# Kernel tuning notes

Hardware: AMD Instinct MI355X
Metric: run time of the kernel (lower is better)

## Reference

```python
import jax, jax.numpy as jnp
import numpy as np

N = 4096       # nodes
E = 131072     # edges (avg degree 32)
IN_C = 512
HID = 512
OUT_C = 64
RANK = 64      # svd_q
N_DOM = 4
EPS = 1e-5     # BatchNorm eps


def setup_inputs() -> dict:
    key = jax.random.key(0)
    ks = jax.random.split(key, 12)
    x = jax.random.normal(ks[0], (N, IN_C), dtype=jnp.float32)
    row = jax.random.randint(ks[1], (E,), 0, N)
    off = jax.random.randint(ks[2], (E,), 1, N)
    col = (row + off) % N  # guarantee no pre-existing self loops
    edge_index = jnp.stack([row, col]).astype(jnp.int32)
    edge_weight = jax.random.uniform(ks[3], (E,), dtype=jnp.float32)
    y = jax.random.randint(ks[4], (N,), 0, N_DOM).astype(jnp.int32)
    W1 = jax.random.normal(ks[5], (IN_C, HID), dtype=jnp.float32) / np.sqrt(IN_C).astype(np.float32)
    b1 = jnp.zeros((HID,), jnp.float32)
    Wmu = jax.random.normal(ks[6], (HID, OUT_C), dtype=jnp.float32) / np.sqrt(HID).astype(np.float32)
    bmu = jnp.zeros((OUT_C,), jnp.float32)
    Wlv = jax.random.normal(ks[7], (HID, OUT_C), dtype=jnp.float32) / np.sqrt(HID).astype(np.float32)
    blv = jnp.zeros((OUT_C,), jnp.float32)
    gamma = jnp.ones((N_DOM, HID), jnp.float32)   # per-domain BN weight
    beta = jnp.zeros((N_DOM, HID), jnp.float32)   # per-domain BN bias
    return dict(x=x, edge_index=edge_index, edge_weight=edge_weight, y=y,
                W1=W1, b1=b1, Wmu=Wmu, bmu=bmu, Wlv=Wlv, blv=blv,
                gamma=gamma, beta=beta)


def _safe_rsqrt(deg):
    # PyG gcn_norm: deg^-0.5 with inf (and here non-positive) masked to 0
    safe = jnp.where(deg > 0, deg, 1.0)
    return jnp.where(deg > 0, 1.0 / jnp.sqrt(safe), 0.0)


def gcn_conv_edges(x, W, b, row, col, w, n):
    # GCNConv with edge weights: add remaining self loops (fill=1), symmetric norm
    loop = jnp.arange(n, dtype=row.dtype)
    row_f = jnp.concatenate([row, loop])
    col_f = jnp.concatenate([col, loop])
    w_f = jnp.concatenate([w, jnp.ones((n,), w.dtype)])
    deg = jax.ops.segment_sum(w_f, col_f, num_segments=n)
    dinv = _safe_rsqrt(deg)
    norm = dinv[row_f] * w_f * dinv[col_f]
    xw = x @ W                                   # [n, out]
    out = jax.ops.segment_sum(norm[:, None] * xw[row_f], col_f, num_segments=n)
    return out + b


def gcn_conv_dense(x, W, b, A):
    # Dense-adjacency GCNConv (reconstructed adjacency already has a diagonal,
    # so add_remaining_self_loops is a no-op). deg over target (col) index.
    deg = A.sum(axis=0)
    dinv = _safe_rsqrt(deg)
    Ahat = dinv[:, None] * A * dinv[None, :]     # [n, n] normalized
    return Ahat.T @ (x @ W) + b                  # aggregate at targets


def svd_lowrank_recon(A, q, niter=2):
    # torch.svd_lowrank-style randomized SVD, then U @ diag(s) @ V^T
    omega = jax.random.normal(jax.random.key(42), (A.shape[1], q), A.dtype)
    Qb = jnp.linalg.qr(A @ omega)[0]
    for _ in range(niter):
        Qb = jnp.linalg.qr(A.T @ Qb)[0]
        Qb = jnp.linalg.qr(A @ Qb)[0]
    B = Qb.T @ A                                 # [q, n]
    U, s, Vt = jnp.linalg.svd(B, full_matrices=False)
    return (Qb @ (U * s)) @ Vt                   # [n, n] low-rank reconstruction


def dsbn_relu(x, y, gamma, beta):
    # Domain-specific BatchNorm (training-mode batch stats per domain) + ReLU
    out = jnp.zeros_like(x)
    for i in range(N_DOM):
        m = (y == i)
        mf = m.astype(x.dtype)[:, None]
        cnt = jnp.maximum(mf.sum(), 1.0)
        mean = (x * mf).sum(0) / cnt
        var = (((x - mean) ** 2) * mf).sum(0) / cnt   # biased var, as BatchNorm
        xn = (x - mean) / jnp.sqrt(var + EPS) * gamma[i] + beta[i]
        out = jnp.where(m[:, None], xn, out)
    return jax.nn.relu(out)


def reference(x, edge_index, edge_weight, y, W1, b1, Wmu, bmu, Wlv, blv, gamma, beta):
    row, col = edge_index[0], edge_index[1]
    # ----- branch 1: original sparse graph -----
    h1 = dsbn_relu(gcn_conv_edges(x, W1, b1, row, col, edge_weight, N), y, gamma, beta)
    z_mean1 = gcn_conv_edges(h1, Wmu, bmu, row, col, edge_weight, N)
    z_log1 = gcn_conv_edges(h1, Wlv, blv, row, col, edge_weight, N)
    # ----- branch 2: SVD low-rank reconstructed (dense) graph -----
    A = jnp.zeros((N, N), x.dtype).at[row, col].add(edge_weight)  # coalesced COO
    A2 = svd_lowrank_recon(A, RANK)
    h2 = dsbn_relu(gcn_conv_dense(x, W1, b1, A2), y, gamma, beta)
    z_mean2 = gcn_conv_dense(h2, Wmu, bmu, A2)
    z_log2 = gcn_conv_dense(h2, Wlv, blv, A2)
    return (z_mean1, z_log1, z_mean2, z_log2)
```

## Files before the change

### kernel.cpp

```cpp
#include <hip/hip_runtime.h>
#include <hip/hip_bf16.h>


#define NN    4096
#define NEDG  131072
#define INC   512
#define HIDC  512
#define OUTC  64
#define RK    64
#define NDOM  4
#define EPSBN 1e-5f

typedef unsigned short ushortT;
typedef __attribute__((ext_vector_type(8))) short bf16x8;
typedef __attribute__((ext_vector_type(4))) float f32x4;

static inline int cdiv(int a, int b){ return (a + b - 1) / b; }

__device__ __forceinline__ float bf2f(unsigned u){ return __uint_as_float(u << 16); }

__global__ __launch_bounds__(256) void k_detect(const unsigned short* __restrict__ p,
                                                int* __restrict__ flag){
  int t = threadIdx.x;
  int cnt = 0;
  for (int i = t; i < 4096; i += 256){
    unsigned short v = p[2*i];
    int e = (v >> 7) & 0xFF;
    if (e >= 100 && e <= 140) cnt++;
  }
  __shared__ int sh[256];
  sh[t] = cnt; __syncthreads();
  for (int off = 128; off > 0; off >>= 1){ if (t < off) sh[t] += sh[t+off]; __syncthreads(); }
  if (t == 0) *flag = (sh[0] >= 2048) ? 0 : 1;
}

__device__ __forceinline__ float upc1(const void* s, int f, int off){
  return f ? ((const float*)s)[off]
           : __bfloat162float(((const __hip_bfloat16*)s)[off]);
}
__device__ __forceinline__ ushortT tobf(float v){
  __hip_bfloat16 h = __float2bfloat16(v);
  return *(ushortT*)&h;
}
#define SEG_X   2097152
#define SEG_W1  262144
#define SEG_W   131072
#define SEG_WMU 32768
#define SEG_GB  2048
#define SEG_B1  512
#define SEG_BO  64
#define OFF1 (SEG_X)
#define OFF2 (OFF1+SEG_W1)
#define OFF3 (OFF2+SEG_W)
#define OFF4 (OFF3+SEG_WMU)
#define OFF5 (OFF4+SEG_WMU)
#define OFF6 (OFF5+SEG_GB)
#define OFF7 (OFF6+SEG_GB)
#define OFF8 (OFF7+SEG_B1)
#define OFF9 (OFF8+SEG_BO)
#define OFFT (OFF9+SEG_BO)

__global__ __launch_bounds__(256) void k_upcast_all(
    const void* x, const void* W1, const void* w, const void* Wmu, const void* Wlv,
    const void* gm, const void* bt, const void* b1, const void* bmu, const void* blv,
    const int* __restrict__ isf32,
    float* dx, float* dW1, float* dw, float* dWmu, float* dWlv,
    float* dgm, float* dbt, float* db1, float* dbmu, float* dblv,
    ushortT* xbf, ushortT* W1bf, ushortT* Wmubf, ushortT* Wlvbf){
  int i = blockIdx.x*256 + threadIdx.x;
  if (i >= OFFT) return;
  int f = *isf32;
  if      (i < OFF1){ float v = upc1(x, f, i); dx[i] = v; xbf[i] = tobf(v); }
  else if (i < OFF2){ float v = upc1(W1, f, i - OFF1); dW1[i - OFF1] = v; W1bf[i - OFF1] = tobf(v); }
  else if (i < OFF3) dw  [i - OFF2] = upc1(w,   f, i - OFF2);
  else if (i < OFF4){ float v = upc1(Wmu, f, i - OFF3); dWmu[i - OFF3] = v; Wmubf[i - OFF3] = tobf(v); }
  else if (i < OFF5){ float v = upc1(Wlv, f, i - OFF4); dWlv[i - OFF4] = v; Wlvbf[i - OFF4] = tobf(v); }
  else if (i < OFF6) dgm [i - OFF5] = upc1(gm,  f, i - OFF5);
  else if (i < OFF7) dbt [i - OFF6] = upc1(bt,  f, i - OFF6);
  else if (i < OFF8) db1 [i - OFF7] = upc1(b1,  f, i - OFF7);
  else if (i < OFF9) dbmu[i - OFF8] = upc1(bmu, f, i - OFF8);
  else               dblv[i - OFF9] = upc1(blv, f, i - OFF9);
}

__global__ __launch_bounds__(256) void k_fill(float* d, float v, int n){
  int i = blockIdx.x*256 + threadIdx.x;
  if (i < n) d[i] = v;
}
__global__ __launch_bounds__(256) void k_filld(double* d, double v, int n){
  int i = blockIdx.x*256 + threadIdx.x;
  if (i < n) d[i] = v;
}
__global__ __launch_bounds__(256) void k_prep(float* deg, int* cntR, int* cntC, int* dcnt){
  int i = blockIdx.x*256 + threadIdx.x;
  if (i < NN){ deg[i] = 1.0f; cntR[i] = 0; cntC[i] = 0; }
  if (i < NDOM) dcnt[i] = 0;
}
__global__ __launch_bounds__(256) void k_f64to32x2(const double* __restrict__ s0, float* __restrict__ d0,
                                                   const double* __restrict__ s1, float* __restrict__ d1,
                                                   int n){
  int i = blockIdx.x*256 + threadIdx.x;
  if (i < n){ d0[i] = (float)s0[i]; d1[i] = (float)s1[i]; }
}

__global__ __launch_bounds__(256) void k_hist(const int* __restrict__ row, const int* __restrict__ col,
                                              const float* __restrict__ w, float* deg,
                                              int* cntR, int* cntC){
  int e = blockIdx.x*256 + threadIdx.x;
  if (e < NEDG){
    atomicAdd(&deg[col[e]], w[e]);
    atomicAdd(&cntR[row[e]], 1);
    atomicAdd(&cntC[col[e]], 1);
  }
}
__global__ __launch_bounds__(256) void k_dinv(const float* deg, float* dinv, int n){
  int i = blockIdx.x*256 + threadIdx.x;
  if (i < n){ float d = deg[i]; dinv[i] = (d > 0.f) ? 1.f/sqrtf(d) : 0.f; }
}
__global__ __launch_bounds__(256) void k_norm1(const int* __restrict__ row, const int* __restrict__ col,
                                               const float* __restrict__ w, const float* __restrict__ dinv,
                                               float* __restrict__ nrm){
  int e = blockIdx.x*256 + threadIdx.x;
  if (e < NEDG) nrm[e] = dinv[row[e]] * w[e] * dinv[col[e]];
}
__global__ __launch_bounds__(1024) void k_scan4096(const int* __restrict__ cnt,
                                                   int* __restrict__ ptr, int* __restrict__ pos){
  __shared__ int sh[1024];
  int t = threadIdx.x;
  int b = t*4;
  int a0 = cnt[b], a1 = cnt[b+1], a2 = cnt[b+2], a3 = cnt[b+3];
  sh[t] = a0 + a1 + a2 + a3;
  __syncthreads();
  for (int off = 1; off < 1024; off <<= 1){
    int v = (t >= off) ? sh[t-off] : 0;
    __syncthreads();
    sh[t] += v;
    __syncthreads();
  }
  int excl = (t == 0) ? 0 : sh[t-1];
  ptr[b]   = excl;            pos[b]   = excl;
  ptr[b+1] = excl+a0;         pos[b+1] = excl+a0;
  ptr[b+2] = excl+a0+a1;      pos[b+2] = excl+a0+a1;
  ptr[b+3] = excl+a0+a1+a2;   pos[b+3] = excl+a0+a1+a2;
  if (t == 1023) ptr[4096] = sh[1023];
}
__global__ __launch_bounds__(256) void k_scatter(const int* __restrict__ row, const int* __restrict__ col,
                                                 int* posR, int* posC, int* eidR, int* eidC){
  int e = blockIdx.x*256 + threadIdx.x;
  if (e < NEDG){
    int p = atomicAdd(&posR[row[e]], 1); eidR[p] = e;
    int q = atomicAdd(&posC[col[e]], 1); eidC[q] = e;
  }
}
__global__ __launch_bounds__(256) void k_edges(const int* __restrict__ rowA, const int* __restrict__ colA,
        const float* __restrict__ wf, const float* __restrict__ nrm,
        const int* __restrict__ eidR, const int* __restrict__ eidC,
        int* __restrict__ csrSrc, float* __restrict__ csrW,
        int* __restrict__ cscSrc, float* __restrict__ cscW, float* __restrict__ cscN){
  int p = blockIdx.x*256 + threadIdx.x;
  if (p < NEDG){
    int eR = eidR[p]; csrSrc[p] = colA[eR]; csrW[p] = wf[eR];
    int eC = eidC[p]; cscSrc[p] = rowA[eC]; cscW[p] = wf[eC]; cscN[p] = nrm[eC];
  }
}
__global__ __launch_bounds__(256) void k_dcnt(const int* __restrict__ y, int* dcnt){
  int i = blockIdx.x*256 + threadIdx.x;
  if (i < NN) atomicAdd(&dcnt[y[i]], 1);
}

__device__ __forceinline__ unsigned rotl32(unsigned x, unsigned d){ return (x << d) | (x >> (32u - d)); }
#define TF_ROUND4(R0,R1,R2,R3) \
  x0 += x1; x1 = rotl32(x1,R0); x1 ^= x0; \
  x0 += x1; x1 = rotl32(x1,R1); x1 ^= x0; \
  x0 += x1; x1 = rotl32(x1,R2); x1 ^= x0; \
  x0 += x1; x1 = rotl32(x1,R3); x1 ^= x0;

__device__ __forceinline__ void tf2x32(unsigned k0, unsigned k1, unsigned c0, unsigned c1,
                                       unsigned* o0, unsigned* o1){
  unsigned ks2 = 0x1BD11BDAu ^ k0 ^ k1;
  unsigned x0 = c0 + k0, x1 = c1 + k1;
  TF_ROUND4(13,15,26,6);   x0 += k1;  x1 += ks2 + 1u;
  TF_ROUND4(17,29,16,24);  x0 += ks2; x1 += k0 + 2u;
  TF_ROUND4(13,15,26,6);   x0 += k0;  x1 += k1 + 3u;
  TF_ROUND4(17,29,16,24);  x0 += k1;  x1 += ks2 + 4u;
  TF_ROUND4(13,15,26,6);   x0 += ks2; x1 += k0 + 5u;
  *o0 = x0; *o1 = x1;
}

__device__ double erfinv64(double x){
  double w = -log1p(-x*x);
  double p;
  if (w < 5.0){
    w -= 2.5;
    p = 2.81022636e-08;  p = p*w + 3.43273939e-07; p = p*w - 3.5233877e-06;
    p = p*w - 4.39150654e-06; p = p*w + 0.00021858087; p = p*w - 0.00125372503;
    p = p*w - 0.00417768164;  p = p*w + 0.246640727;   p = p*w + 1.50140941;
  } else {
    w = sqrt(w) - 3.0;
    p = -0.000200214257; p = p*w + 0.000100950558; p = p*w + 0.00134934322;
    p = p*w - 0.00367342844; p = p*w + 0.00573950773; p = p*w - 0.0076224613;
    p = p*w + 0.00943887047; p = p*w + 1.00167406;    p = p*w + 2.83297682;
  }
  double y = p * x;
  const double c = 1.1283791670955126;
  #pragma unroll
  for (int it = 0; it < 3; it++){
    double err = erf(y) - x;
    y -= err / (c * exp(-y*y));
  }
  return y;
}

__device__ float bits_to_normal(unsigned b){
  float f = __uint_as_float((b >> 9) | 0x3f800000u) - 1.0f;
  const float lo = -0.99999994f;
  float x = fmaxf(lo, f * 2.0f + lo);
  double r = 1.4142135623730951 * erfinv64((double)x);
  return (float)r;
}

__global__ __launch_bounds__(256) void k_omega(float* __restrict__ om){
  int i = blockIdx.x*256 + threadIdx.x;
  if (i >= 262144) return;
  unsigned o0, o1;
  tf2x32(0u, 42u, 0u, (unsigned)i, &o0, &o1);
  om[i] = bits_to_normal(o0 ^ o1);
}

__global__ __launch_bounds__(256) void k_gemm_bf16(
    const ushortT* __restrict__ A, const ushortT* __restrict__ B,
    float* __restrict__ Cc, ushortT* __restrict__ Cbf){
  __shared__ ushortT As2[64][40];
  __shared__ ushortT Bs2[64][40];
  int t = threadIdx.x;
  int bm = blockIdx.y * 64, bn = blockIdx.x * 64;
  int w = t >> 6, l = t & 63;
  int lr = l & 15, lk = l >> 4;
  f32x4 acc[4] = {};
  int ar = t >> 2, ac = (t & 3) * 8;
  int bc = t & 63, bk = (t >> 6) * 8;
  for (int k0 = 0; k0 < 512; k0 += 32){
    *(uint4*)&As2[ar][ac] = *(const uint4*)&A[(size_t)(bm + ar) * 512 + k0 + ac];
    ushortT tmp[8];
    #pragma unroll
    for (int j = 0; j < 8; j++)
      tmp[j] = B[(size_t)(k0 + bk + j) * 512 + bn + bc];
    *(uint4*)&Bs2[bc][bk] = *(uint4*)tmp;
    __syncthreads();
    bf16x8 afrag = *(bf16x8*)&As2[w * 16 + lr][lk * 8];
    #pragma unroll
    for (int nt = 0; nt < 4; nt++){
      bf16x8 bfrag = *(bf16x8*)&Bs2[nt * 16 + lr][lk * 8];
      acc[nt] = __builtin_amdgcn_mfma_f32_16x16x32_bf16(afrag, bfrag, acc[nt], 0, 0, 0);
    }
    __syncthreads();
  }
  #pragma unroll
  for (int nt = 0; nt < 4; nt++){
    #pragma unroll
    for (int i = 0; i < 4; i++){
      size_t idx = (size_t)(bm + w * 16 + lk * 4 + i) * 512 + bn + nt * 16 + lr;
      float v = acc[nt][i];
      Cc[idx] = v;
      Cbf[idx] = tobf(v);
    }
  }
}

__global__ __launch_bounds__(256) void k_gemm_hw(
    const ushortT* __restrict__ A, const ushortT* __restrict__ B,
    float* __restrict__ Cc){
  __shared__ ushortT As2[64][40];
  __shared__ ushortT Bs2[64][40];
  int t = threadIdx.x;
  int bm = blockIdx.x * 64;
  int w = t >> 6, l = t & 63;
  int lr = l & 15, lk = l >> 4;
  f32x4 acc[4] = {};
  int ar = t >> 2, ac = (t & 3) * 8;
  int bc = t & 63, bk = (t >> 6) * 8;
  for (int k0 = 0; k0 < 512; k0 += 32){
    *(uint4*)&As2[ar][ac] = *(const uint4*)&A[(size_t)(bm + ar) * 512 + k0 + ac];
    ushortT tmp[8];
    #pragma unroll
    for (int j = 0; j < 8; j++)
      tmp[j] = B[(size_t)(k0 + bk + j) * 64 + bc];
    *(uint4*)&Bs2[bc][bk] = *(uint4*)tmp;
    __syncthreads();
    bf16x8 afrag = *(bf16x8*)&As2[w * 16 + lr][lk * 8];
    #pragma unroll
    for (int nt = 0; nt < 4; nt++){
      bf16x8 bfrag = *(bf16x8*)&Bs2[nt * 16 + lr][lk * 8];
      acc[nt] = __builtin_amdgcn_mfma_f32_16x16x32_bf16(afrag, bfrag, acc[nt], 0, 0, 0);
    }
    __syncthreads();
  }
  #pragma unroll
  for (int nt = 0; nt < 4; nt++){
    #pragma unroll
    for (int i = 0; i < 4; i++){
      Cc[(size_t)(bm + w * 16 + lk * 4 + i) * 64 + nt * 16 + lr] = acc[nt][i];
    }
  }
}

__global__ __launch_bounds__(256) void k_gemm_nn(int M, int Nn, int K,
      const float* __restrict__ A, int lda, const float* __restrict__ B, int ldb,
      float* __restrict__ Cc, int ldc, const float* __restrict__ rowscale,
      const float* __restrict__ kscale, const float* __restrict__ bias){
  __shared__ float As[16][65];
  __shared__ float Bs[16][65];
  int bm = blockIdx.y*64, bn = blockIdx.x*64;
  int t = threadIdx.x;
  int tr = t >> 4, tc = t & 15;
  float acc[4][4] = {};
  for (int k0 = 0; k0 < K; k0 += 16){
    #pragma unroll
    for (int q = 0; q < 4; q++){
      int idx = t*4 + q;
      int m = idx >> 4, kk = idx & 15;
      As[kk][m] = A[(size_t)(bm+m)*lda + (k0+kk)];
    }
    #pragma unroll
    for (int q = 0; q < 4; q++){
      int idx = t + q*256;
      int kk = idx >> 6, n = idx & 63;
      float ks = kscale ? kscale[k0+kk] : 1.0f;
      Bs[kk][n] = B[(size_t)(k0+kk)*ldb + (bn+n)] * ks;
    }
    __syncthreads();
    #pragma unroll
    for (int kk = 0; kk < 16; kk++){
      float a0 = As[kk][tr*4+0], a1 = As[kk][tr*4+1], a2 = As[kk][tr*4+2], a3 = As[kk][tr*4+3];
      float b0 = Bs[kk][tc*4+0], b1 = Bs[kk][tc*4+1], b2 = Bs[kk][tc*4+2], b3 = Bs[kk][tc*4+3];
      acc[0][0] += a0*b0; acc[0][1] += a0*b1; acc[0][2] += a0*b2; acc[0][3] += a0*b3;
      acc[1][0] += a1*b0; acc[1][1] += a1*b1; acc[1][2] += a1*b2; acc[1][3] += a1*b3;
      acc[2][0] += a2*b0; acc[2][1] += a2*b1; acc[2][2] += a2*b2; acc[2][3] += a2*b3;
      acc[3][0] += a3*b0; acc[3][1] += a3*b1; acc[3][2] += a3*b2; acc[3][3] += a3*b3;
    }
    __syncthreads();
  }
  #pragma unroll
  for (int i2 = 0; i2 < 4; i2++){
    int m = bm + tr*4 + i2;
    float rs = rowscale ? rowscale[m] : 1.0f;
    #pragma unroll
    for (int j2 = 0; j2 < 4; j2++){
      int n = bn + tc*4 + j2;
      float v = acc[i2][j2] * rs;
      if (bias) v += bias[n];
      Cc[(size_t)m*ldc + n] = v;
    }
  }
}

__global__ __launch_bounds__(256) void k_gemm_tn_sk(int M, int Nn, int K, int kchunk,
      const float* __restrict__ A, int lda, const float* __restrict__ B, int ldb,
      float* __restrict__ Cc, int ldc, const float* __restrict__ kscale){
  __shared__ float As[32][17];
  __shared__ float Bs[32][17];
  int bm = blockIdx.y*16, bn = blockIdx.x*16;
  int kb = blockIdx.z*kchunk, ke = kb + kchunk;
  int t = threadIdx.x;
  int tm = t >> 4, tn = t & 15;
  float acc = 0.f;
  for (int k0 = kb; k0 < ke; k0 += 32){
    #pragma unroll
    for (int q = 0; q < 2; q++){
      int idx = t + q*256;
      int kk = idx >> 4, m = idx & 15;
      float sv = kscale ? kscale[k0+kk] : 1.0f;
      As[kk][m] = A[(size_t)(k0+kk)*lda + (bm+m)] * sv;
      Bs[kk][m] = B[(size_t)(k0+kk)*ldb + (bn+m)];
    }
    __syncthreads();
    #pragma unroll
    for (int kk = 0; kk < 32; kk++) acc += As[kk][tm] * Bs[kk][tn];
    __syncthreads();
  }
  atomicAdd(&Cc[(size_t)(bm+tm)*ldc + (bn+tn)], acc);
}

__global__ __launch_bounds__(64) void k_spmm32(const int* __restrict__ ptr,
                       const int* __restrict__ src, const float* __restrict__ cf,
                       const float* __restrict__ X, float* __restrict__ Y){
  int seg = blockIdx.x;
  int t = threadIdx.x;
  double acc = 0.0;
  int p0 = ptr[seg], p1 = ptr[seg+1];
  for (int p = p0; p < p1; ++p){
    acc += (double)cf[p] * (double)X[(size_t)src[p]*RK + t];
  }
  Y[(size_t)seg*RK + t] = (float)acc;
}
__global__ __launch_bounds__(64) void k_spmm32to64(const int* __restrict__ ptr,
                       const int* __restrict__ src, const float* __restrict__ cf,
                       const float* __restrict__ X, double* __restrict__ Y){
  int seg = blockIdx.x;
  int t = threadIdx.x;
  double acc = 0.0;
  int p0 = ptr[seg], p1 = ptr[seg+1];
  for (int p = p0; p < p1; ++p){
    acc += (double)cf[p] * (double)X[(size_t)src[p]*RK + t];
  }
  Y[(size_t)seg*RK + t] = acc;
}
__global__ __launch_bounds__(64) void k_spmm64(const int* __restrict__ ptr,
                       const int* __restrict__ src, const float* __restrict__ cf,
                       const double* __restrict__ X, double* __restrict__ Y){
  int seg = blockIdx.x;
  int t = threadIdx.x;
  double acc = 0.0;
  int p0 = ptr[seg], p1 = ptr[seg+1];
  for (int p = p0; p < p1; ++p){
    acc += (double)cf[p] * X[(size_t)src[p]*RK + t];
  }
  Y[(size_t)seg*RK + t] = acc;
}
__global__ __launch_bounds__(256) void k_gram64(const double* __restrict__ X, double* __restrict__ G){
  __shared__ double Xs[64][65];
  int b = blockIdx.x;
  int t = threadIdx.x;
  #pragma unroll
  for (int q = 0; q < 16; q++){
    int idx = t + q*256;
    Xs[idx >> 6][idx & 63] = X[(size_t)(b*64 + (idx >> 6))*RK + (idx & 63)];
  }
  __syncthreads();
  int i = t >> 2;
  int j0 = (t & 3) * 16;
  double acc[16];
  #pragma unroll
  for (int jj = 0; jj < 16; jj++) acc[jj] = 0.0;
  for (int k = 0; k < 64; k++){
    double a = Xs[k][i];
    #pragma unroll
    for (int jj = 0; jj < 16; jj++) acc[jj] += a * Xs[k][j0+jj];
  }
  #pragma unroll
  for (int jj = 0; jj < 16; jj++) atomicAdd(&G[i*RK + j0 + jj], acc[jj]);
}
#define CHOL_CHUNK(I0) \
  for (int k2 = 0; k2 < 16; k2++){ \
    int k = (I0) + k2; \
    int buf = k & 1; \
    if (j == k){ \
      double d = sqrt(fmax(cdiag, 1e-300)); \
      double s = 1.0 / d; \
      myd = d; \
      sdd[k] = s; \
      _Pragma("unroll") \
      for (int i = (I0); i < 64; i++){ c[i] *= s; colk[buf][i] = c[i]; } \
    } \
    __syncthreads(); \
    if (j > k){ \
      double cj = colk[buf][j]; \
      cdiag -= cj * cj; \
      _Pragma("unroll") \
      for (int i = (I0); i < 64; i++){ c[i] -= colk[buf][i] * cj; } \
    } \
    __syncthreads(); \
  }

__global__ __launch_bounds__(64) void k_chol64(double* __restrict__ G, double* __restrict__ sdd){
  __shared__ double colk[2][64];
  int j = threadIdx.x;
  double c[64];
  #pragma unroll
  for (int i = 0; i < 64; i++) c[i] = G[i*64 + j];
  double cdiag = 0.0, myd = 0.0;
  #pragma unroll
  for (int i = 0; i < 64; i++) if (i == j) cdiag = c[i];
  CHOL_CHUNK(0)
  CHOL_CHUNK(16)
  CHOL_CHUNK(32)
  CHOL_CHUNK(48)
  #pragma unroll
  for (int i = 0; i < 64; i++){
    double v = (i > j) ? c[i] : 0.0;
    if (i == j) v = myd;
    G[i*64 + j] = v;
  }
}
__global__ __launch_bounds__(256) void k_trinv64(const double* __restrict__ L,
      const double* __restrict__ sdd, double* __restrict__ Rinv){
  __shared__ double gl[64][65];
  __shared__ double Xl[64][65];
  __shared__ double sdinv[64];
  __shared__ double Sl[3][16][17];
  int t = threadIdx.x;
  #pragma unroll
  for (int q = 0; q < 16; q++){
    int idx = t + (q << 8);
    gl[idx >> 6][idx & 63] = L[idx];
  }
  if (t < 64) sdinv[t] = sdd[t];
  for (int idx = t; idx < 64*65; idx += 256)
    ((double*)Xl)[idx] = 0.0;
  __syncthreads();
  if (t < 64){
    int b = t >> 4, c2 = t & 15;
    int g0 = b << 4;
    int gc = g0 + c2;
    Xl[gc][gc] = sdinv[gc];
    for (int i = c2 - 1; i >= 0; i--){
      int gi = g0 + i;
      double s = 0.0;
      for (int k2 = i + 1; k2 <= c2; k2++)
        s += gl[g0 + k2][gi] * Xl[g0 + k2][gc];
      Xl[gi][gc] = -s * sdinv[gi];
    }
  }
  __syncthreads();
  for (int d = 1; d < 4; d++){
    int np = 4 - d;
    int tot = np << 8;
    for (int e = t; e < tot; e += 256){
      int p = e >> 8;
      int i = (e >> 4) & 15, jj = e & 15;
      int gi = (p << 4) + i, gj = ((p + d) << 4) + jj;
      double s = 0.0;
      int a0 = (p + 1) << 4, a1 = (p + d + 1) << 4;
      for (int a = a0; a < a1; a++)
        s += gl[a][gi] * Xl[a][gj];
      Sl[p][i][jj] = s;
    }
    __syncthreads();
    for (int e = t; e < tot; e += 256){
      int p = e >> 8;
      int i = (e >> 4) & 15, jj = e & 15;
      int gi = (p << 4) + i, gj = ((p + d) << 4) + jj;
      double s = 0.0;
      #pragma unroll
      for (int k2 = 0; k2 < 16; k2++)
        s += Xl[gi][(p << 4) + k2] * Sl[p][k2][jj];
      Xl[gi][gj] = -s;
    }
    __syncthreads();
  }
  #pragma unroll
  for (int q = 0; q < 16; q++){
    int e2 = t + (q << 8);
    Rinv[e2] = Xl[e2 >> 6][e2 & 63];
  }
}
__global__ __launch_bounds__(256) void k_applyR64(const double* __restrict__ src,
      const double* __restrict__ Rinv, double* __restrict__ dst){
  __shared__ double Rs[64][65];
  int t = threadIdx.x;
  #pragma unroll
  for (int q = 0; q < 16; q++){
    int idx = t + q*256;
    Rs[idx >> 6][idx & 63] = Rinv[idx];
  }
  __syncthreads();
  int r = blockIdx.x*4 + (t >> 6);
  int j = t & 63;
  const double* rowp = src + (size_t)r*RK;
  double s = 0.0;
  for (int k = 0; k <= j; k++) s += rowp[k] * Rs[k][j];
  dst[(size_t)r*RK + j] = s;
}
__global__ __launch_bounds__(256) void k_qsum64(const double* __restrict__ Q, double* __restrict__ qs){
  int j = blockIdx.x;  int t = threadIdx.x;
  double a = 0.0;
  for (int n = t; n < NN; n += 256) a += Q[(size_t)n*RK + j];
  __shared__ double sh[256];
  sh[t] = a; __syncthreads();
  for (int off = 128; off > 0; off >>= 1){ if (t < off) sh[t] += sh[t+off]; __syncthreads(); }
  if (t == 0) qs[j] = sh[0];
}
__global__ __launch_bounds__(256) void k_deg2f(const double* __restrict__ C, const double* __restrict__ qs,
                                               float* __restrict__ dinv2){
  int i = blockIdx.x*256 + threadIdx.x;
  if (i >= NN) return;
  double s = 0.0;
  #pragma unroll
  for (int k = 0; k < RK; k++) s += C[(size_t)i*RK + k] * qs[k];
  dinv2[i] = (s > 0.0) ? (float)(1.0/sqrt(s)) : 0.f;
}

__global__ __launch_bounds__(256) void k_spmm_bf16(const int* __restrict__ ptr,
        const int* __restrict__ src, const float* __restrict__ cf,
        const ushortT* __restrict__ Xb, float* __restrict__ Y,
        const float* __restrict__ self_dinv, const float* __restrict__ bias){
  int seg = blockIdx.x;
  int t = threadIdx.x;
  float acc0, acc1;
  {
    float sd = self_dinv[seg]; float s2 = sd*sd;
    unsigned v = *(const unsigned*)&Xb[(size_t)seg*HIDC + 2*t];
    acc0 = s2 * bf2f(v & 0xffffu);
    acc1 = s2 * bf2f(v >> 16);
  }
  int p0 = ptr[seg], p1 = ptr[seg+1];
  for (int p = p0; p < p1; ++p){
    int o = src[p];
    float c = cf[p];
    unsigned v = *(const unsigned*)&Xb[(size_t)o*HIDC + 2*t];
    acc0 += c * bf2f(v & 0xffffu);
    acc1 += c * bf2f(v >> 16);
  }
  acc0 += bias[2*t];
  acc1 += bias[2*t+1];
  Y[(size_t)seg*HIDC + 2*t]     = acc0;
  Y[(size_t)seg*HIDC + 2*t + 1] = acc1;
}
__global__ void k_spmm(const int* __restrict__ ptr, const int* __restrict__ src,
                       const float* __restrict__ cf,
                       const float* __restrict__ X, int ldx,
                       float* __restrict__ Y, int ldy,
                       const float* __restrict__ self_dinv, const float* __restrict__ bias){
  int seg = blockIdx.x;
  int t = threadIdx.x;
  float acc0 = 0.f;
  {
    float sd = self_dinv[seg];
    acc0 = sd*sd * X[(size_t)seg*ldx + t];
  }
  int p0 = ptr[seg], p1 = ptr[seg+1];
  for (int p = p0; p < p1; ++p){
    acc0 += cf[p] * X[(size_t)src[p]*ldx + t];
  }
  acc0 += bias[t];
  Y[(size_t)seg*ldy + t] = acc0;
}

__global__ __launch_bounds__(256) void k_bnstats(const float* __restrict__ H, const int* __restrict__ y,
        const int* __restrict__ dcnt, const float* __restrict__ gamma, const float* __restrict__ beta,
        float* __restrict__ scal, float* __restrict__ shft){
  int j = blockIdx.x;
  int t = threadIdx.x;
  float s0=0,s1=0,s2=0,s3=0,q0=0,q1=0,q2=0,q3=0;
  for (int n = t; n < NN; n += 256){
    float v = H[(size_t)n*HIDC + j];
    int d = y[n];
    float v2 = v*v;
    if      (d == 0){ s0 += v; q0 += v2; }
    else if (d == 1){ s1 += v; q1 += v2; }
    else if (d == 2){ s2 += v; q2 += v2; }
    else            { s3 += v; q3 += v2; }
  }
  __shared__ float sh[256][8];
  sh[t][0]=s0; sh[t][1]=s1; sh[t][2]=s2; sh[t][3]=s3;
  sh[t][4]=q0; sh[t][5]=q1; sh[t][6]=q2; sh[t][7]=q3;
  __syncthreads();
  for (int off = 128; off > 0; off >>= 1){
    if (t < off){
      #pragma unroll
      for (int q = 0; q < 8; q++) sh[t][q] += sh[t+off][q];
    }
    __syncthreads();
  }
  if (t < NDOM){
    float cnt  = fmaxf((float)dcnt[t], 1.0f);
    float mean = sh[0][t] / cnt;
    float var  = fmaxf(sh[0][4+t] / cnt - mean*mean, 0.f);
    float inv  = 1.0f / sqrtf(var + EPSBN);
    float gmm  = gamma[t*HIDC + j];
    scal[t*HIDC + j] = gmm * inv;
    shft[t*HIDC + j] = beta[t*HIDC + j] - mean * gmm * inv;
  }
}
__global__ __launch_bounds__(256) void k_bnapply(float* __restrict__ H, const int* __restrict__ y,
        const float* __restrict__ scal, const float* __restrict__ shft,
        ushortT* __restrict__ Hbf){
  int idx = blockIdx.x*256 + threadIdx.x;
  if (idx >= NN*HIDC) return;
  int n = idx >> 9, j = idx & (HIDC-1);
  int d = y[n];
  float v = H[idx] * scal[d*HIDC + j] + shft[d*HIDC + j];
  v = v > 0.f ? v : 0.f;
  H[idx] = v;
  Hbf[idx] = tobf(v);
}

extern "C" void kernel_launch(void* const* d_in, const int* in_sizes, int n_in,
                              void* d_out, int out_size, void* d_ws, size_t ws_size,
                              hipStream_t stream){
  (void)in_sizes; (void)n_in; (void)out_size;
  const void* x_in  = d_in[0];
  const int*  ei    = (const int*)d_in[1];
  const void* w_in  = d_in[2];
  const int*  yv    = (const int*)d_in[3];
  const void* W1i   = d_in[4];
  const void* b1i   = d_in[5];
  const void* Wmui  = d_in[6];
  const void* bmui  = d_in[7];
  const void* Wlvi  = d_in[8];
  const void* blvi  = d_in[9];
  const void* gmi   = d_in[10];
  const void* bti   = d_in[11];
  const int* rowA = ei;
  const int* colA = ei + NEDG;
  float* zout = (float*)d_out;

  double* Dp = (double*)d_ws;
  size_t od = 0;
  double* Qd0 = Dp + od; od += (size_t)NN*RK;
  double* Qd1 = Dp + od; od += (size_t)NN*RK;
  double* Cd  = Dp + od; od += (size_t)NN*RK;
  double* Gd  = Dp + od; od += RK*RK;
  double* Rid = Dp + od; od += RK*RK;
  double* qsd = Dp + od; od += RK;
  double* sdd = Dp + od; od += RK;
  float* Fp = (float*)(Dp + od);
  size_t o = 0;
  float* xf   = Fp + o; o += (size_t)NN*INC;
  float* W1f  = Fp + o; o += (size_t)INC*HIDC;
  float* b1f  = Fp + o; o += HIDC;
  float* Wmuf = Fp + o; o += (size_t)HIDC*OUTC;
  float* bmuf = Fp + o; o += OUTC;
  float* Wlvf = Fp + o; o += (size_t)HIDC*OUTC;
  float* blvf = Fp + o; o += OUTC;
  float* gmf  = Fp + o; o += NDOM*HIDC;
  float* btf  = Fp + o; o += NDOM*HIDC;
  float* wf   = Fp + o; o += NEDG;
  float* xw1  = Fp + o; o += (size_t)NN*HIDC;
  float* hwA  = Fp + o; o += (size_t)NN*OUTC;
  float* hwB  = Fp + o; o += (size_t)NN*OUTC;
  float* Bf1  = Fp + o; o += (size_t)NN*RK;
  float* Cm   = Fp + o; o += (size_t)NN*RK;
  float* Qf0  = Fp + o; o += (size_t)NN*RK;
  float* Qf1  = Fp + o; o += (size_t)NN*RK;
  float* Tm   = Fp + o; o += (size_t)RK*HIDC;
  float* Umu  = Fp + o; o += RK*RK;
  float* deg1 = Fp + o; o += NN;
  float* dinv1= Fp + o; o += NN;
  float* dinv2= Fp + o; o += NN;
  float* norm1= Fp + o; o += NEDG;
  float* scal = Fp + o; o += NDOM*HIDC;
  float* shft = Fp + o; o += NDOM*HIDC;
  float* csrW = Fp + o; o += NEDG;
  float* cscW = Fp + o; o += NEDG;
  float* cscN = Fp + o; o += NEDG;
  ushortT* xbf   = (ushortT*)(Fp + o); o += (size_t)NN*INC/2;
  ushortT* W1bf  = (ushortT*)(Fp + o); o += (size_t)INC*HIDC/2;
  ushortT* xw1bf = (ushortT*)(Fp + o); o += (size_t)NN*HIDC/2;
  ushortT* Wmubf = (ushortT*)(Fp + o); o += (size_t)HIDC*OUTC/2;
  ushortT* Wlvbf = (ushortT*)(Fp + o); o += (size_t)HIDC*OUTC/2;
  int* Ip = (int*)(Fp + o);
  size_t oi = 0;
  int* cntR = Ip + oi; oi += NN;
  int* ptrR = Ip + oi; oi += NN + 1;
  int* posR = Ip + oi; oi += NN;
  int* eidR = Ip + oi; oi += NEDG;
  int* cntC = Ip + oi; oi += NN;
  int* ptrC = Ip + oi; oi += NN + 1;
  int* posC = Ip + oi; oi += NN;
  int* eidC = Ip + oi; oi += NEDG;
  int* csrSrc = Ip + oi; oi += NEDG;
  int* cscSrc = Ip + oi; oi += NEDG;
  int* dcnt = Ip + oi; oi += NDOM;
  int* dflag= Ip + oi; oi += 1;

  size_t need = od*sizeof(double) + o*sizeof(float) + (oi+16)*sizeof(int);
  if (ws_size < need) return;

  float* hbuf = xf;

  const int T = 256;
  k_detect<<<1,T,0,stream>>>((const unsigned short*)x_in, dflag);
  k_upcast_all<<<cdiv(OFFT,T),T,0,stream>>>(
      x_in, W1i, w_in, Wmui, Wlvi, gmi, bti, b1i, bmui, blvi, dflag,
      xf, W1f, wf, Wmuf, Wlvf, gmf, btf, b1f, bmuf, blvf,
      xbf, W1bf, Wmubf, Wlvbf);

  k_prep<<<cdiv(NN,T),T,0,stream>>>(deg1, cntR, cntC, dcnt);
  k_hist <<<cdiv(NEDG,T),T,0,stream>>>(rowA, colA, wf, deg1, cntR, cntC);
  k_dinv <<<cdiv(NN,T),T,0,stream>>>(deg1, dinv1, NN);
  k_norm1<<<cdiv(NEDG,T),T,0,stream>>>(rowA, colA, wf, dinv1, norm1);
  k_scan4096<<<1,1024,0,stream>>>(cntR, ptrR, posR);
  k_scan4096<<<1,1024,0,stream>>>(cntC, ptrC, posC);
  k_scatter<<<cdiv(NEDG,T),T,0,stream>>>(rowA, colA, posR, posC, eidR, eidC);
  k_edges<<<cdiv(NEDG,T),T,0,stream>>>(rowA, colA, wf, norm1, eidR, eidC,
                                       csrSrc, csrW, cscSrc, cscW, cscN);
  k_omega<<<cdiv(NN*RK,T),T,0,stream>>>(Qf0);
  k_dcnt <<<cdiv(NN,T),T,0,stream>>>(yv, dcnt);

  k_gemm_bf16<<<dim3(HIDC/64, NN/64),256,0,stream>>>(xbf, W1bf, xw1, xw1bf);
  k_spmm_bf16<<<NN,256,0,stream>>>(ptrC, cscSrc, cscN, xw1bf, hbuf, dinv1, b1f);
  k_bnstats<<<HIDC,256,0,stream>>>(hbuf, yv, dcnt, gmf, btf, scal, shft);
  k_bnapply<<<cdiv(NN*HIDC,T),T,0,stream>>>(hbuf, yv, scal, shft, xw1bf);
  k_gemm_hw<<<NN/64,256,0,stream>>>(xw1bf, Wmubf, hwA);
  k_gemm_hw<<<NN/64,256,0,stream>>>(xw1bf, Wlvbf, hwB);
  k_spmm<<<NN,64,0,stream>>>(ptrC, cscSrc, cscN, hwA,OUTC, zout + 0*NN*OUTC,OUTC, dinv1, bmuf);
  k_spmm<<<NN,64,0,stream>>>(ptrC, cscSrc, cscN, hwB,OUTC, zout + 1*NN*OUTC,OUTC, dinv1, blvf);

  k_spmm32<<<NN,64,0,stream>>>(ptrR, csrSrc, csrW, Qf0, Qf1);
  k_spmm32<<<NN,64,0,stream>>>(ptrC, cscSrc, cscW, Qf1, Qf0);
  k_spmm32<<<NN,64,0,stream>>>(ptrR, csrSrc, csrW, Qf0, Qf1);
  k_spmm32<<<NN,64,0,stream>>>(ptrC, cscSrc, cscW, Qf1, Qf0);
  k_spmm32to64<<<NN,64,0,stream>>>(ptrR, csrSrc, csrW, Qf0, Qd1);
  k_filld<<<cdiv(RK*RK,T),T,0,stream>>>(Gd, 0.0, RK*RK);
  k_gram64<<<NN/64,256,0,stream>>>(Qd1, Gd);
  k_chol64<<<1,64,0,stream>>>(Gd, sdd);
  k_trinv64<<<1,256,0,stream>>>(Gd, sdd, Rid);
  k_applyR64<<<NN/4,256,0,stream>>>(Qd1, Rid, Qd0);
  k_spmm64<<<NN,64,0,stream>>>(ptrC, cscSrc, cscW, Qd0, Cd);
  k_qsum64<<<RK,256,0,stream>>>(Qd0, qsd);
  k_deg2f<<<cdiv(NN,T),T,0,stream>>>(Cd, qsd, dinv2);
  k_f64to32x2<<<cdiv(NN*RK,T),T,0,stream>>>(Qd0, Bf1, Cd, Cm, NN*RK);

  k_fill<<<cdiv(RK*HIDC,T),T,0,stream>>>(Tm, 0.f, RK*HIDC);
  k_gemm_tn_sk<<<dim3(HIDC/16, RK/16, 8),256,0,stream>>>(RK,HIDC,NN,512, Bf1,RK, xw1,HIDC, Tm,HIDC, dinv2);
  k_gemm_nn<<<dim3(HIDC/64, NN/64),256,0,stream>>>(NN,HIDC,RK, Cm,RK, Tm,HIDC, hbuf,HIDC, dinv2, nullptr, b1f);
  k_bnstats<<<HIDC,256,0,stream>>>(hbuf, yv, dcnt, gmf, btf, scal, shft);
  k_bnapply<<<cdiv(NN*HIDC,T),T,0,stream>>>(hbuf, yv, scal, shft, xw1bf);
  k_gemm_hw<<<NN/64,256,0,stream>>>(xw1bf, Wmubf, hwA);
  k_gemm_hw<<<NN/64,256,0,stream>>>(xw1bf, Wlvbf, hwB);
  k_fill<<<cdiv(RK*RK,T),T,0,stream>>>(Umu, 0.f, RK*RK);
  k_gemm_tn_sk<<<dim3(RK/16, RK/16, 16),256,0,stream>>>(RK,RK,NN,256, Bf1,RK, hwA,OUTC, Umu,RK, dinv2);
  k_gemm_nn<<<dim3(1, NN/64),256,0,stream>>>(NN,OUTC,RK, Cm,RK, Umu,RK, zout + 2*NN*OUTC,OUTC, dinv2, nullptr, bmuf);
  k_fill<<<cdiv(RK*RK,T),T,0,stream>>>(Umu, 0.f, RK*RK);
  k_gemm_tn_sk<<<dim3(RK/16, RK/16, 16),256,0,stream>>>(RK,RK,NN,256, Bf1,RK, hwB,OUTC, Umu,RK, dinv2);
  k_gemm_nn<<<dim3(1, NN/64),256,0,stream>>>(NN,OUTC,RK, Cm,RK, Umu,RK, zout + 3*NN*OUTC,OUTC, dinv2, nullptr, blvf);
}
```

Measured before the change: 650.4 us.

## Merge paired mu/logvar kernels and overlap the Cholesky with the branch-1 SpMM

Several paired launches become single launches. The mu and logvar GEMMs, SpMMs, split-K and NN GEMMs each become one grid that picks its operands by block index. The degree-inverse computation is folded into the f64-to-f32 conversion. The single-block Cholesky is placed in the same launch as the branch-1 bf16 SpMM, so the serial factorisation runs alongside useful work instead of leaving the GPU idle. The branch-1 post-processing is moved after the SVD chain and writes to a new hbf buffer, so xw1bf is no longer overwritten. Launch count and idle tail time drop, at the cost of branchy kernels and more scratch memory.

```diff
diff --git a/kernel.cpp b/kernel.cpp
--- a/kernel.cpp
+++ b/kernel.cpp
@@ -95,11 +95,17 @@
   if (i < NN){ deg[i] = 1.0f; cntR[i] = 0; cntC[i] = 0; }
   if (i < NDOM) dcnt[i] = 0;
 }
-__global__ __launch_bounds__(256) void k_f64to32x2(const double* __restrict__ s0, float* __restrict__ d0,
-                                                   const double* __restrict__ s1, float* __restrict__ d1,
-                                                   int n){
+__global__ __launch_bounds__(256) void k_fin(const double* __restrict__ Qd,
+        float* __restrict__ Bf1, const double* __restrict__ Cd, float* __restrict__ Cm,
+        const double* __restrict__ qs, float* __restrict__ dinv2){
   int i = blockIdx.x*256 + threadIdx.x;
-  if (i < n){ d0[i] = (float)s0[i]; d1[i] = (float)s1[i]; }
+  if (i < NN*RK){ Bf1[i] = (float)Qd[i]; Cm[i] = (float)Cd[i]; }
+  if (i < NN){
+    double s = 0.0;
+    #pragma unroll
+    for (int k = 0; k < RK; k++) s += Cd[(size_t)i*RK + k] * qs[k];
+    dinv2[i] = (s > 0.0) ? (float)(1.0/sqrt(s)) : 0.f;
+  }
 }
 
 __global__ __launch_bounds__(256) void k_hist(const int* __restrict__ row, const int* __restrict__ col,
@@ -266,13 +272,17 @@
   }
 }
 
-__global__ __launch_bounds__(256) void k_gemm_hw(
-    const ushortT* __restrict__ A, const ushortT* __restrict__ B,
-    float* __restrict__ Cc){
+__global__ __launch_bounds__(256) void k_gemm_hw2(
+    const ushortT* __restrict__ A, const ushortT* __restrict__ Bm,
+    const ushortT* __restrict__ Bl, float* __restrict__ Ca, float* __restrict__ Cb){
   __shared__ ushortT As2[64][40];
   __shared__ ushortT Bs2[64][40];
   int t = threadIdx.x;
-  int bm = blockIdx.x * 64;
+  int nb = NN/64;
+  int second = blockIdx.x >= nb;
+  int bm = (blockIdx.x - (second ? nb : 0)) * 64;
+  const ushortT* B = second ? Bl : Bm;
+  float* Cc = second ? Cb : Ca;
   int w = t >> 6, l = t & 63;
   int lr = l & 15, lk = l >> 4;
   f32x4 acc[4] = {};
@@ -353,6 +363,59 @@
   }
 }
 
+__global__ __launch_bounds__(256) void k_gemm_nn2(
+      const float* __restrict__ A,
+      const float* __restrict__ Um,
+      const float* __restrict__ rowscale,
+      const float* __restrict__ bmu, const float* __restrict__ blv,
+      float* __restrict__ zout){
+  __shared__ float As[16][65];
+  __shared__ float Bs[16][65];
+  int z = blockIdx.z;
+  const float* B = Um + (size_t)z*RK*RK;
+  const float* bias = z ? blv : bmu;
+  float* Cc = zout + (size_t)(2+z)*NN*OUTC;
+  int bm = blockIdx.y*64;
+  int t = threadIdx.x;
+  int tr = t >> 4, tc = t & 15;
+  float acc[4][4] = {};
+  for (int k0 = 0; k0 < RK; k0 += 16){
+    #pragma unroll
+    for (int q = 0; q < 4; q++){
+      int idx = t*4 + q;
+      int m = idx >> 4, kk = idx & 15;
+      As[kk][m] = A[(size_t)(bm+m)*RK + (k0+kk)];
+    }
+    #pragma unroll
+    for (int q = 0; q < 4; q++){
+      int idx = t + q*256;
+      int kk = idx >> 6, n = idx & 63;
+      Bs[kk][n] = B[(size_t)(k0+kk)*RK + n];
+    }
+    __syncthreads();
+    #pragma unroll
+    for (int kk = 0; kk < 16; kk++){
+      float a0 = As[kk][tr*4+0], a1 = As[kk][tr*4+1], a2 = As[kk][tr*4+2], a3 = As[kk][tr*4+3];
+      float b0 = Bs[kk][tc*4+0], b1 = Bs[kk][tc*4+1], b2 = Bs[kk][tc*4+2], b3 = Bs[kk][tc*4+3];
+      acc[0][0] += a0*b0; acc[0][1] += a0*b1; acc[0][2] += a0*b2; acc[0][3] += a0*b3;
+      acc[1][0] += a1*b0; acc[1][1] += a1*b1; acc[1][2] += a1*b2; acc[1][3] += a1*b3;
+      acc[2][0] += a2*b0; acc[2][1] += a2*b1; acc[2][2] += a2*b2; acc[2][3] += a2*b3;
+      acc[3][0] += a3*b0; acc[3][1] += a3*b1; acc[3][2] += a3*b2; acc[3][3] += a3*b3;
+    }
+    __syncthreads();
+  }
+  #pragma unroll
+  for (int i2 = 0; i2 < 4; i2++){
+    int m = bm + tr*4 + i2;
+    float rs = rowscale[m];
+    #pragma unroll
+    for (int j2 = 0; j2 < 4; j2++){
+      int n = tc*4 + j2;
+      Cc[(size_t)m*OUTC + n] = acc[i2][j2] * rs + bias[n];
+    }
+  }
+}
+
 __global__ __launch_bounds__(256) void k_gemm_tn_sk(int M, int Nn, int K, int kchunk,
       const float* __restrict__ A, int lda, const float* __restrict__ B, int ldb,
       float* __restrict__ Cc, int ldc, const float* __restrict__ kscale){
@@ -380,6 +443,38 @@
   atomicAdd(&Cc[(size_t)(bm+tm)*ldc + (bn+tn)], acc);
 }
 
+__global__ __launch_bounds__(256) void k_gemm_tn_sk2(
+      const float* __restrict__ A,
+      const float* __restrict__ Ba, const float* __restrict__ Bb,
+      float* __restrict__ Um,
+      const float* __restrict__ kscale){
+  __shared__ float As[32][17];
+  __shared__ float Bs[32][17];
+  int z = blockIdx.z;
+  int second = z >= 16;
+  int kb = (second ? z - 16 : z) * 256, ke = kb + 256;
+  const float* B = second ? Bb : Ba;
+  float* Cc = Um + (second ? RK*RK : 0);
+  int bm = blockIdx.y*16, bn = blockIdx.x*16;
+  int t = threadIdx.x;
+  int tm = t >> 4, tn = t & 15;
+  float acc = 0.f;
+  for (int k0 = kb; k0 < ke; k0 += 32){
+    #pragma unroll
+    for (int q = 0; q < 2; q++){
+      int idx = t + q*256;
+      int kk = idx >> 4, m = idx & 15;
+      As[kk][m] = A[(size_t)(k0+kk)*RK + (bm+m)] * kscale[k0+kk];
+      Bs[kk][m] = B[(size_t)(k0+kk)*OUTC + (bn+m)];
+    }
+    __syncthreads();
+    #pragma unroll
+    for (int kk = 0; kk < 32; kk++) acc += As[kk][tm] * Bs[kk][tn];
+    __syncthreads();
+  }
+  atomicAdd(&Cc[(size_t)(bm+tm)*RK + (bn+tn)], acc);
+}
+
 __global__ __launch_bounds__(64) void k_spmm32(const int* __restrict__ ptr,
                        const int* __restrict__ src, const float* __restrict__ cf,
                        const float* __restrict__ X, float* __restrict__ Y){
@@ -439,11 +534,12 @@
   #pragma unroll
   for (int jj = 0; jj < 16; jj++) atomicAdd(&G[i*RK + j0 + jj], acc[jj]);
 }
-#define CHOL_CHUNK(I0) \
+
+#define CHOLF_CHUNK(I0) \
   for (int k2 = 0; k2 < 16; k2++){ \
     int k = (I0) + k2; \
     int buf = k & 1; \
-    if (j == k){ \
+    if (t < 64 && j == k){ \
       double d = sqrt(fmax(cdiag, 1e-300)); \
       double s = 1.0 / d; \
       myd = d; \
@@ -452,7 +548,7 @@
       for (int i = (I0); i < 64; i++){ c[i] *= s; colk[buf][i] = c[i]; } \
     } \
     __syncthreads(); \
-    if (j > k){ \
+    if (t < 64 && j > k && j < 64){ \
       double cj = colk[buf][j]; \
       cdiag -= cj * cj; \
       _Pragma("unroll") \
@@ -461,26 +557,59 @@
     __syncthreads(); \
   }
 
-__global__ __launch_bounds__(64) void k_chol64(double* __restrict__ G, double* __restrict__ sdd){
+__global__ __launch_bounds__(256) void k_chol_spmm(
+    double* __restrict__ G, double* __restrict__ sdd,
+    const int* __restrict__ ptr, const int* __restrict__ src, const float* __restrict__ cf,
+    const ushortT* __restrict__ Xb, float* __restrict__ Y,
+    const float* __restrict__ self_dinv, const float* __restrict__ bias){
   __shared__ double colk[2][64];
-  int j = threadIdx.x;
-  double c[64];
-  #pragma unroll
-  for (int i = 0; i < 64; i++) c[i] = G[i*64 + j];
-  double cdiag = 0.0, myd = 0.0;
-  #pragma unroll
-  for (int i = 0; i < 64; i++) if (i == j) cdiag = c[i];
-  CHOL_CHUNK(0)
-  CHOL_CHUNK(16)
-  CHOL_CHUNK(32)
-  CHOL_CHUNK(48)
-  #pragma unroll
-  for (int i = 0; i < 64; i++){
-    double v = (i > j) ? c[i] : 0.0;
-    if (i == j) v = myd;
-    G[i*64 + j] = v;
-  }
-}
+  int t = threadIdx.x;
+  if (blockIdx.x == 0){
+    int j = t;
+    double c[64];
+    double cdiag = 0.0, myd = 0.0;
+    if (t < 64){
+      #pragma unroll
+      for (int i = 0; i < 64; i++) c[i] = G[i*64 + j];
+      #pragma unroll
+      for (int i = 0; i < 64; i++) if (i == j) cdiag = c[i];
+    }
+    CHOLF_CHUNK(0)
+    CHOLF_CHUNK(16)
+    CHOLF_CHUNK(32)
+    CHOLF_CHUNK(48)
+    if (t < 64){
+      #pragma unroll
+      for (int i = 0; i < 64; i++){
+        double v = (i > j) ? c[i] : 0.0;
+        if (i == j) v = myd;
+        G[i*64 + j] = v;
+      }
+    }
+  } else {
+    int seg = blockIdx.x - 1;
+    float acc0, acc1;
+    {
+      float sd = self_dinv[seg]; float s2 = sd*sd;
+      unsigned v = *(const unsigned*)&Xb[(size_t)seg*HIDC + 2*t];
+      acc0 = s2 * bf2f(v & 0xffffu);
+      acc1 = s2 * bf2f(v >> 16);
+    }
+    int p0 = ptr[seg], p1 = ptr[seg+1];
+    for (int p = p0; p < p1; ++p){
+      int o = src[p];
+      float cc = cf[p];
+      unsigned v = *(const unsigned*)&Xb[(size_t)o*HIDC + 2*t];
+      acc0 += cc * bf2f(v & 0xffffu);
+      acc1 += cc * bf2f(v >> 16);
+    }
+    acc0 += bias[2*t];
+    acc1 += bias[2*t+1];
+    Y[(size_t)seg*HIDC + 2*t]     = acc0;
+    Y[(size_t)seg*HIDC + 2*t + 1] = acc1;
+  }
+}
+
 __global__ __launch_bounds__(256) void k_trinv64(const double* __restrict__ L,
       const double* __restrict__ sdd, double* __restrict__ Rinv){
   __shared__ double gl[64][65];
@@ -569,60 +698,31 @@
   for (int off = 128; off > 0; off >>= 1){ if (t < off) sh[t] += sh[t+off]; __syncthreads(); }
   if (t == 0) qs[j] = sh[0];
 }
-__global__ __launch_bounds__(256) void k_deg2f(const double* __restrict__ C, const double* __restrict__ qs,
-                                               float* __restrict__ dinv2){
-  int i = blockIdx.x*256 + threadIdx.x;
-  if (i >= NN) return;
-  double s = 0.0;
-  #pragma unroll
-  for (int k = 0; k < RK; k++) s += C[(size_t)i*RK + k] * qs[k];
-  dinv2[i] = (s > 0.0) ? (float)(1.0/sqrt(s)) : 0.f;
-}
-
-__global__ __launch_bounds__(256) void k_spmm_bf16(const int* __restrict__ ptr,
-        const int* __restrict__ src, const float* __restrict__ cf,
-        const ushortT* __restrict__ Xb, float* __restrict__ Y,
-        const float* __restrict__ self_dinv, const float* __restrict__ bias){
-  int seg = blockIdx.x;
-  int t = threadIdx.x;
-  float acc0, acc1;
+
+__global__ void k_spmm2(const int* __restrict__ ptr, const int* __restrict__ src,
+                        const float* __restrict__ cf,
+                        const float* __restrict__ Xa, const float* __restrict__ Xb2,
+                        float* __restrict__ zout,
+                        const float* __restrict__ self_dinv,
+                        const float* __restrict__ bmu, const float* __restrict__ blv){
+  int b = blockIdx.x;
+  int second = b >= NN;
+  int seg = second ? b - NN : b;
+  const float* X = second ? Xb2 : Xa;
+  const float* bias = second ? blv : bmu;
+  float* Y = zout + (second ? (size_t)NN*OUTC : 0);
+  int t = threadIdx.x;
+  float acc0;
   {
-    float sd = self_dinv[seg]; float s2 = sd*sd;
-    unsigned v = *(const unsigned*)&Xb[(size_t)seg*HIDC + 2*t];
-    acc0 = s2 * bf2f(v & 0xffffu);
-    acc1 = s2 * bf2f(v >> 16);
+    float sd = self_dinv[seg];
+    acc0 = sd*sd * X[(size_t)seg*OUTC + t];
   }
   int p0 = ptr[seg], p1 = ptr[seg+1];
   for (int p = p0; p < p1; ++p){
-    int o = src[p];
-    float c = cf[p];
-    unsigned v = *(const unsigned*)&Xb[(size_t)o*HIDC + 2*t];
-    acc0 += c * bf2f(v & 0xffffu);
-    acc1 += c * bf2f(v >> 16);
-  }
-  acc0 += bias[2*t];
-  acc1 += bias[2*t+1];
-  Y[(size_t)seg*HIDC + 2*t]     = acc0;
-  Y[(size_t)seg*HIDC + 2*t + 1] = acc1;
-}
-__global__ void k_spmm(const int* __restrict__ ptr, const int* __restrict__ src,
-                       const float* __restrict__ cf,
-                       const float* __restrict__ X, int ldx,
-                       float* __restrict__ Y, int ldy,
-                       const float* __restrict__ self_dinv, const float* __restrict__ bias){
-  int seg = blockIdx.x;
-  int t = threadIdx.x;
-  float acc0 = 0.f;
-  {
-    float sd = self_dinv[seg];
-    acc0 = sd*sd * X[(size_t)seg*ldx + t];
-  }
-  int p0 = ptr[seg], p1 = ptr[seg+1];
-  for (int p = p0; p < p1; ++p){
-    acc0 += cf[p] * X[(size_t)src[p]*ldx + t];
+    acc0 += cf[p] * X[(size_t)src[p]*OUTC + t];
   }
   acc0 += bias[t];
-  Y[(size_t)seg*ldy + t] = acc0;
+  Y[(size_t)seg*OUTC + t] = acc0;
 }
 
 __global__ __launch_bounds__(256) void k_bnstats(const float* __restrict__ H, const int* __restrict__ y,
@@ -723,7 +823,7 @@
   float* Qf0  = Fp + o; o += (size_t)NN*RK;
   float* Qf1  = Fp + o; o += (size_t)NN*RK;
   float* Tm   = Fp + o; o += (size_t)RK*HIDC;
-  float* Umu  = Fp + o; o += RK*RK;
+  float* Umu  = Fp + o; o += 2*RK*RK;
   float* deg1 = Fp + o; o += NN;
   float* dinv1= Fp + o; o += NN;
   float* dinv2= Fp + o; o += NN;
@@ -736,6 +836,7 @@
   ushortT* xbf   = (ushortT*)(Fp + o); o += (size_t)NN*INC/2;
   ushortT* W1bf  = (ushortT*)(Fp + o); o += (size_t)INC*HIDC/2;
   ushortT* xw1bf = (ushortT*)(Fp + o); o += (size_t)NN*HIDC/2;
+  ushortT* hbf   = (ushortT*)(Fp + o); o += (size_t)NN*HIDC/2;
   ushortT* Wmubf = (ushortT*)(Fp + o); o += (size_t)HIDC*OUTC/2;
   ushortT* Wlvbf = (ushortT*)(Fp + o); o += (size_t)HIDC*OUTC/2;
   int* Ip = (int*)(Fp + o);
@@ -778,13 +879,6 @@
   k_dcnt <<<cdiv(NN,T),T,0,stream>>>(yv, dcnt);
 
   k_gemm_bf16<<<dim3(HIDC/64, NN/64),256,0,stream>>>(xbf, W1bf, xw1, xw1bf);
-  k_spmm_bf16<<<NN,256,0,stream>>>(ptrC, cscSrc, cscN, xw1bf, hbuf, dinv1, b1f);
-  k_bnstats<<<HIDC,256,0,stream>>>(hbuf, yv, dcnt, gmf, btf, scal, shft);
-  k_bnapply<<<cdiv(NN*HIDC,T),T,0,stream>>>(hbuf, yv, scal, shft, xw1bf);
-  k_gemm_hw<<<NN/64,256,0,stream>>>(xw1bf, Wmubf, hwA);
-  k_gemm_hw<<<NN/64,256,0,stream>>>(xw1bf, Wlvbf, hwB);
-  k_spmm<<<NN,64,0,stream>>>(ptrC, cscSrc, cscN, hwA,OUTC, zout + 0*NN*OUTC,OUTC, dinv1, bmuf);
-  k_spmm<<<NN,64,0,stream>>>(ptrC, cscSrc, cscN, hwB,OUTC, zout + 1*NN*OUTC,OUTC, dinv1, blvf);
 
   k_spmm32<<<NN,64,0,stream>>>(ptrR, csrSrc, csrW, Qf0, Qf1);
   k_spmm32<<<NN,64,0,stream>>>(ptrC, cscSrc, cscW, Qf1, Qf0);
@@ -793,25 +887,28 @@
   k_spmm32to64<<<NN,64,0,stream>>>(ptrR, csrSrc, csrW, Qf0, Qd1);
   k_filld<<<cdiv(RK*RK,T),T,0,stream>>>(Gd, 0.0, RK*RK);
   k_gram64<<<NN/64,256,0,stream>>>(Qd1, Gd);
-  k_chol64<<<1,64,0,stream>>>(Gd, sdd);
+
+  k_chol_spmm<<<NN+1,256,0,stream>>>(Gd, sdd, ptrC, cscSrc, cscN, xw1bf, hbuf,
+                                     dinv1, b1f);
+
   k_trinv64<<<1,256,0,stream>>>(Gd, sdd, Rid);
   k_applyR64<<<NN/4,256,0,stream>>>(Qd1, Rid, Qd0);
   k_spmm64<<<NN,64,0,stream>>>(ptrC, cscSrc, cscW, Qd0, Cd);
   k_qsum64<<<RK,256,0,stream>>>(Qd0, qsd);
-  k_deg2f<<<cdiv(NN,T),T,0,stream>>>(Cd, qsd, dinv2);
-  k_f64to32x2<<<cdiv(NN*RK,T),T,0,stream>>>(Qd0, Bf1, Cd, Cm, NN*RK);
+  k_fin<<<cdiv(NN*RK,T),T,0,stream>>>(Qd0, Bf1, Cd, Cm, qsd, dinv2);
+
+  k_bnstats<<<HIDC,256,0,stream>>>(hbuf, yv, dcnt, gmf, btf, scal, shft);
+  k_bnapply<<<cdiv(NN*HIDC,T),T,0,stream>>>(hbuf, yv, scal, shft, hbf);
+  k_gemm_hw2<<<2*(NN/64),256,0,stream>>>(hbf, Wmubf, Wlvbf, hwA, hwB);
+  k_spmm2<<<2*NN,64,0,stream>>>(ptrC, cscSrc, cscN, hwA, hwB, zout, dinv1, bmuf, blvf);
 
   k_fill<<<cdiv(RK*HIDC,T),T,0,stream>>>(Tm, 0.f, RK*HIDC);
   k_gemm_tn_sk<<<dim3(HIDC/16, RK/16, 8),256,0,stream>>>(RK,HIDC,NN,512, Bf1,RK, xw1,HIDC, Tm,HIDC, dinv2);
   k_gemm_nn<<<dim3(HIDC/64, NN/64),256,0,stream>>>(NN,HIDC,RK, Cm,RK, Tm,HIDC, hbuf,HIDC, dinv2, nullptr, b1f);
   k_bnstats<<<HIDC,256,0,stream>>>(hbuf, yv, dcnt, gmf, btf, scal, shft);
-  k_bnapply<<<cdiv(NN*HIDC,T),T,0,stream>>>(hbuf, yv, scal, shft, xw1bf);
-  k_gemm_hw<<<NN/64,256,0,stream>>>(xw1bf, Wmubf, hwA);
-  k_gemm_hw<<<NN/64,256,0,stream>>>(xw1bf, Wlvbf, hwB);
-  k_fill<<<cdiv(RK*RK,T),T,0,stream>>>(Umu, 0.f, RK*RK);
-  k_gemm_tn_sk<<<dim3(RK/16, RK/16, 16),256,0,stream>>>(RK,RK,NN,256, Bf1,RK, hwA,OUTC, Umu,RK, dinv2);
-  k_gemm_nn<<<dim3(1, NN/64),256,0,stream>>>(NN,OUTC,RK, Cm,RK, Umu,RK, zout + 2*NN*OUTC,OUTC, dinv2, nullptr, bmuf);
-  k_fill<<<cdiv(RK*RK,T),T,0,stream>>>(Umu, 0.f, RK*RK);
-  k_gemm_tn_sk<<<dim3(RK/16, RK/16, 16),256,0,stream>>>(RK,RK,NN,256, Bf1,RK, hwB,OUTC, Umu,RK, dinv2);
-  k_gemm_nn<<<dim3(1, NN/64),256,0,stream>>>(NN,OUTC,RK, Cm,RK, Umu,RK, zout + 3*NN*OUTC,OUTC, dinv2, nullptr, blvf);
-}
+  k_bnapply<<<cdiv(NN*HIDC,T),T,0,stream>>>(hbuf, yv, scal, shft, hbf);
+  k_gemm_hw2<<<2*(NN/64),256,0,stream>>>(hbf, Wmubf, Wlvbf, hwA, hwB);
+  k_fill<<<cdiv(2*RK*RK,T),T,0,stream>>>(Umu, 0.f, 2*RK*RK);
+  k_gemm_tn_sk2<<<dim3(RK/16, RK/16, 32),256,0,stream>>>(Bf1, hwA, hwB, Umu, dinv2);
+  k_gemm_nn2<<<dim3(1, NN/64, 2),256,0,stream>>>(Cm, Umu, dinv2, bmuf, blvf, zout);
+}
```

After: 578.1 us. -11.1%, faster.
